# Performance work log

Measured on AMD Instinct MI355X. Metric: run time of the kernel, lower is better.

The kernel has to match this reference:

```python
import jax, jax.numpy as jnp
import numpy as np

N = 100000
E = 3200000
IN_DIM = 500
HID = 64
OUT_DIM = 40
K = 10
ALPHA = 0.1
BN_EPS = 1e-5


def setup_inputs() -> dict:
    key = jax.random.key(0)
    ks = jax.random.split(key, 10)
    x = jax.random.normal(ks[0], (N, IN_DIM), dtype=jnp.float32)
    edge_index = jax.random.randint(ks[1], (2, E), 0, N, dtype=jnp.int64)
    W1 = jax.random.normal(ks[2], (IN_DIM, HID), dtype=jnp.float32) / np.sqrt(IN_DIM)
    b1 = jnp.zeros((HID,), dtype=jnp.float32)
    bn_gamma = jnp.ones((HID,), dtype=jnp.float32)
    bn_beta = jnp.zeros((HID,), dtype=jnp.float32)
    bn_mean = jax.random.normal(ks[3], (HID,), dtype=jnp.float32) * 0.1
    bn_var = jax.random.uniform(ks[4], (HID,), dtype=jnp.float32) + 0.5
    W2 = jax.random.normal(ks[5], (HID, OUT_DIM), dtype=jnp.float32) / np.sqrt(HID)
    b2 = jnp.zeros((OUT_DIM,), dtype=jnp.float32)
    return {"x": x, "edge_index": edge_index, "W1": W1, "b1": b1,
            "bn_gamma": bn_gamma, "bn_beta": bn_beta, "bn_mean": bn_mean,
            "bn_var": bn_var, "W2": W2, "b2": b2}


def _gcn_norm(edge_index):
    # PyG gcn_norm with add_self_loops=True, symmetric normalization.
    row = jnp.concatenate([edge_index[0], jnp.arange(N, dtype=edge_index.dtype)])
    col = jnp.concatenate([edge_index[1], jnp.arange(N, dtype=edge_index.dtype)])
    deg = jax.ops.segment_sum(jnp.ones_like(col, dtype=jnp.float32), col, num_segments=N)
    dinv = jnp.where(deg > 0, jax.lax.rsqrt(deg), 0.0)
    norm = dinv[row] * dinv[col]  # [E+N]
    return row, col, norm


def _appnp(x, row, col, norm):
    h = x
    def step(xk, _):
        msg = norm[:, None] * xk[row]                       # [E+N, HID] gather
        agg = jax.ops.segment_sum(msg, col, num_segments=N)  # scatter-add
        return (1.0 - ALPHA) * agg + ALPHA * h, None
    xK, _ = jax.lax.scan(step, x, None, length=K)
    return xK


def reference(x, edge_index, W1, b1, bn_gamma, bn_beta, bn_mean, bn_var, W2, b2):
    row, col, norm = _gcn_norm(edge_index)
    h = x @ W1 + b1                                   # lin1
    h = _appnp(h, row, col, norm)                     # K-step APPNP
    h = (h - bn_mean) * jax.lax.rsqrt(bn_var + BN_EPS) * bn_gamma + bn_beta  # BN (eval)
    # dropout is identity in eval mode
    emb = h @ W2 + b2                                 # lin2
    out = jax.nn.log_softmax(emb, axis=1)
    return out, emb
```

## Files before the change

### kernel.cpp

```cpp
#include <hip/hip_runtime.h>
#include <math.h>

#define N_NODES 100000
#define N_EDGES 3200000
#define IN_DIM  500
#define HID     64
#define OUT_DIM 40
#define K_ITERS 10
#define ALPHA   0.1f
#define BN_EPS  1e-5f

#define PDIM 48
#define NBUCK 782
#define TILE_A 8192

__device__ __forceinline__ void unpack4(uint2 v, float f[4]) {
    f[0] = __uint_as_float(v.x << 16);
    f[1] = __uint_as_float(v.x & 0xffff0000u);
    f[2] = __uint_as_float(v.y << 16);
    f[3] = __uint_as_float(v.y & 0xffff0000u);
}
__device__ __forceinline__ unsigned pack2(float a, float b) {
    unsigned ua = __float_as_uint(a);
    unsigned ub = __float_as_uint(b);
    ua += ((ua >> 16) & 1u) + 0x7fffu;
    ub += ((ub >> 16) & 1u) + 0x7fffu;
    return (ua >> 16) | (ub & 0xffff0000u);
}
__device__ __forceinline__ float edge_w(unsigned e) {
    return __uint_as_float((e >> 17) << 16);
}
__device__ __forceinline__ void fma4(float4& acc, float wgt, const float f[4]) {
    acc.x = fmaf(wgt, f[0], acc.x);
    acc.y = fmaf(wgt, f[1], acc.y);
    acc.z = fmaf(wgt, f[2], acc.z);
    acc.w = fmaf(wgt, f[3], acc.w);
}


__global__ void zero_cnt_kernel(int* __restrict__ cnt) {
    int i = blockIdx.x * 256 + threadIdx.x;
    if (i < N_NODES) cnt[i] = 0;
}

__global__ void hist_kernel(const int* __restrict__ ei, int* __restrict__ cnt) {
    int e = blockIdx.x * 256 + threadIdx.x;
    if (e < N_EDGES) atomicAdd(&cnt[ei[N_EDGES + e]], 1);
}

__global__ void reduce_kernel(const int* __restrict__ cnt, int* __restrict__ psum) {
    __shared__ int s[256];
    int i = blockIdx.x * 256 + threadIdx.x;
    int v = (i < N_NODES) ? cnt[i] : 0;
    s[threadIdx.x] = v;
    __syncthreads();
    for (int off = 128; off > 0; off >>= 1) {
        if (threadIdx.x < (unsigned)off) s[threadIdx.x] += s[threadIdx.x + off];
        __syncthreads();
    }
    if (threadIdx.x == 0) psum[blockIdx.x] = s[0];
}

__global__ void scanp_kernel(const int* __restrict__ psum, int* __restrict__ pexcl,
                             int nparts) {
    __shared__ int s[512];
    int t = threadIdx.x;
    int v = (t < nparts) ? psum[t] : 0;
    s[t] = v;
    __syncthreads();
    for (int off = 1; off < 512; off <<= 1) {
        int tv = (t >= off) ? s[t - off] : 0;
        __syncthreads();
        s[t] += tv;
        __syncthreads();
    }
    if (t < nparts) pexcl[t] = s[t] - v;
}

__global__ void apply_kernel(const int* __restrict__ cnt, const int* __restrict__ pexcl,
                             int* __restrict__ rowptr, float* __restrict__ dinv) {
    __shared__ int s[256];
    int t = threadIdx.x;
    int i = blockIdx.x * 256 + t;
    int v = (i < N_NODES) ? cnt[i] : 0;
    s[t] = v;
    __syncthreads();
    for (int off = 1; off < 256; off <<= 1) {
        int tv = (t >= off) ? s[t - off] : 0;
        __syncthreads();
        s[t] += tv;
        __syncthreads();
    }
    if (i < N_NODES) {
        int excl = pexcl[blockIdx.x] + s[t] - v;
        rowptr[i] = excl;
        dinv[i] = rsqrtf((float)(v + 1));
        if (i == N_NODES - 1) rowptr[N_NODES] = excl + v;
    }
}


__global__ void bcur_init_kernel(const int* __restrict__ rowptr, int* __restrict__ bcursor) {
    int i = blockIdx.x * 256 + threadIdx.x;
    if (i < NBUCK) bcursor[i] = rowptr[i << 7];
}

__global__ __launch_bounds__(256) void bucketA_kernel(const int* __restrict__ ei,
                                                      int* __restrict__ bcursor,
                                                      unsigned* __restrict__ ebuf) {
    __shared__ int cnt[NBUCK];
    __shared__ int gbase[NBUCK];
    for (int i = threadIdx.x; i < NBUCK; i += 256) cnt[i] = 0;
    __syncthreads();
    const int e0 = blockIdx.x * TILE_A;
    const int e1 = (e0 + TILE_A < N_EDGES) ? e0 + TILE_A : N_EDGES;
    for (int e = e0 + threadIdx.x; e < e1; e += 256)
        atomicAdd(&cnt[ei[N_EDGES + e] >> 7], 1);
    __syncthreads();
    for (int i = threadIdx.x; i < NBUCK; i += 256) {
        int n = cnt[i];
        gbase[i] = (n > 0) ? atomicAdd(&bcursor[i], n) : 0;
        cnt[i] = 0;
    }
    __syncthreads();
    for (int e = e0 + threadIdx.x; e < e1; e += 256) {
        int r = ei[e];
        int c = ei[N_EDGES + e];
        int b = c >> 7;
        int rank = atomicAdd(&cnt[b], 1);
        ebuf[gbase[b] + rank] = (unsigned)r | ((unsigned)(c & 127) << 17);
    }
}

__global__ __launch_bounds__(256) void bucketB_kernel(const unsigned* __restrict__ ebuf,
                                                      const int* __restrict__ rowptr,
                                                      const float* __restrict__ dinv,
                                                      unsigned* __restrict__ ew) {
    __shared__ int lcur[128];
    __shared__ float ldinv[128];
    const int base = blockIdx.x << 7;
    const int nn = (N_NODES - base < 128) ? (N_NODES - base) : 128;
    if (threadIdx.x < (unsigned)nn) {
        lcur[threadIdx.x] = rowptr[base + threadIdx.x];
        ldinv[threadIdx.x] = dinv[base + threadIdx.x];
    }
    __syncthreads();
    const int s0 = rowptr[base];
    const int hi = (base + 128 < N_NODES) ? base + 128 : N_NODES;
    const int s1 = rowptr[hi];
    for (int p = s0 + threadIdx.x; p < s1; p += 256) {
        unsigned v = ebuf[p];
        int r = v & 0x1ffff;
        int cl = v >> 17;
        int pos = atomicAdd(&lcur[cl], 1);
        float w = dinv[r] * ldinv[cl];
        unsigned f = __float_as_uint(w) + 0x8000u;
        ew[pos] = (unsigned)r | ((f >> 16) << 17);
    }
}

__global__ void prep_kernel(const float* __restrict__ W2, const float* __restrict__ gamma,
                            const float* __restrict__ beta, const float* __restrict__ mean,
                            const float* __restrict__ var, const float* __restrict__ b1,
                            const float* __restrict__ b2, float* __restrict__ W2p,
                            float* __restrict__ c1, float* __restrict__ cbeta) {
    __shared__ float sc[64];
    __shared__ float sd[64];
    int t = threadIdx.x;
    if (t < 64) {
        float s = rsqrtf(var[t] + BN_EPS) * gamma[t];
        sc[t] = s;
        sd[t] = beta[t] - mean[t] * s;
    }
    __syncthreads();
    for (int i = t; i < 64 * OUT_DIM; i += 256) {
        int f = i / OUT_DIM;
        W2p[i] = sc[f] * W2[i];
    }
    if (t < PDIM) {
        if (t < OUT_DIM) {
            float acb = b2[t], ac1 = 0.f;
            for (int f = 0; f < 64; ++f) {
                float w2 = W2[f * OUT_DIM + t];
                acb = fmaf(sd[f], w2, acb);
                ac1 = fmaf(b1[f] * sc[f], w2, ac1);
            }
            cbeta[t] = acb;
            c1[t] = ac1;
        } else {
            c1[t] = 0.f;
        }
    }
}

__global__ __launch_bounds__(256) void wc_kernel(const float* __restrict__ W1,
                                                 const float* __restrict__ W2p,
                                                 float* __restrict__ Wc) {
    __shared__ float w2s[64 * OUT_DIM];
    for (int i = threadIdx.x; i < 64 * OUT_DIM; i += 256) w2s[i] = W2p[i];
    __syncthreads();
    int idx = blockIdx.x * 256 + threadIdx.x;
    if (idx >= IN_DIM * PDIM) return;
    int k = idx / PDIM, o = idx % PDIM;
    float a = 0.f;
    if (o < OUT_DIM) {
        const float* w1r = W1 + (size_t)k * HID;
#pragma unroll 8
        for (int f = 0; f < 64; ++f) a = fmaf(w1r[f], w2s[f * OUT_DIM + o], a);
    }
    Wc[idx] = a;
}

#define L1_M  128
#define L1_KC 20
#define L1_PITCH 132
__global__ __launch_bounds__(256) void lin1_kernel(const float* __restrict__ x,
                                                   const float* __restrict__ Wc,
                                                   const float* __restrict__ c1,
                                                   float* __restrict__ y0f,
                                                   unsigned* __restrict__ y0b) {
    __shared__ float xsT[L1_KC * L1_PITCH];
    __shared__ float wcs[L1_KC * PDIM];

    const int t = threadIdx.x;
    const int ng = t & 31;
    const int og = t >> 5;
    const int nbase = blockIdx.x * L1_M;

    const int srow = t >> 1;
    const int skb  = (t & 1) * 10;
    const int gsrc = nbase + srow;
    const int gcl  = (gsrc < N_NODES) ? gsrc : (N_NODES - 1);
    const float* xrow = x + (size_t)gcl * IN_DIM;

    float acc[4][6];
#pragma unroll
    for (int i = 0; i < 4; ++i)
#pragma unroll
        for (int j = 0; j < 6; ++j) acc[i][j] = 0.0f;

    for (int k0 = 0; k0 < IN_DIM; k0 += L1_KC) {
        __syncthreads();
#pragma unroll
        for (int u = 0; u < 5; ++u) {
            const float2 xv = *(const float2*)(xrow + k0 + skb + 2 * u);
            xsT[(skb + 2 * u) * L1_PITCH + srow]     = xv.x;
            xsT[(skb + 2 * u + 1) * L1_PITCH + srow] = xv.y;
        }
        for (int i = t; i < L1_KC * PDIM; i += 256) wcs[i] = Wc[(size_t)k0 * PDIM + i];
        __syncthreads();

#pragma unroll 4
        for (int k = 0; k < L1_KC; ++k) {
            const float4 xv = *(const float4*)&xsT[k * L1_PITCH + ng * 4];
            float w[6];
#pragma unroll
            for (int j = 0; j < 6; ++j) w[j] = wcs[k * PDIM + og * 6 + j];
            const float xr[4] = {xv.x, xv.y, xv.z, xv.w};
#pragma unroll
            for (int i = 0; i < 4; ++i)
#pragma unroll
                for (int j = 0; j < 6; ++j)
                    acc[i][j] = fmaf(xr[i], w[j], acc[i][j]);
        }
    }

    float cc[6];
#pragma unroll
    for (int j = 0; j < 6; ++j) cc[j] = c1[og * 6 + j];
#pragma unroll
    for (int i = 0; i < 4; ++i) {
        const int n = nbase + ng * 4 + i;
        if (n < N_NODES) {
            float o[6];
#pragma unroll
            for (int j = 0; j < 6; ++j) o[j] = acc[i][j] + cc[j];
            float* yf = y0f + (size_t)n * PDIM + og * 6;
            *(float2*)(yf)     = make_float2(o[0], o[1]);
            *(float2*)(yf + 2) = make_float2(o[2], o[3]);
            *(float2*)(yf + 4) = make_float2(o[4], o[5]);
            unsigned* yb = y0b + (size_t)n * (PDIM / 2) + og * 3;
            yb[0] = pack2(o[0], o[1]);
            yb[1] = pack2(o[2], o[3]);
            yb[2] = pack2(o[4], o[5]);
        }
    }
}

template <bool LAST>
__global__ __launch_bounds__(256) void appnp40_kernel(const int* __restrict__ rowptr,
                                                      const unsigned* __restrict__ ew,
                                                      const float* __restrict__ dinv,
                                                      const unsigned* __restrict__ yin,
                                                      const float* __restrict__ h,
                                                      unsigned* __restrict__ yout,
                                                      float* __restrict__ yKf) {
    const int sub   = threadIdx.x >> 4;
    const int lane4 = threadIdx.x & 15;
    const int node  = blockIdx.x * 16 + sub;
    const bool act  = lane4 < 10;

    const int beg = rowptr[node];
    const int end = rowptr[node + 1];
    float4 acc = make_float4(0.f, 0.f, 0.f, 0.f);
    int p = beg;
    for (; p + 3 < end; p += 4) {
        const unsigned e0 = ew[p], e1 = ew[p + 1], e2 = ew[p + 2], e3 = ew[p + 3];
        if (act) {
            const uint2 v0 = *(const uint2*)(yin + (size_t)(e0 & 0x1ffff) * (PDIM / 2) + lane4 * 2);
            const uint2 v1 = *(const uint2*)(yin + (size_t)(e1 & 0x1ffff) * (PDIM / 2) + lane4 * 2);
            const uint2 v2 = *(const uint2*)(yin + (size_t)(e2 & 0x1ffff) * (PDIM / 2) + lane4 * 2);
            const uint2 v3 = *(const uint2*)(yin + (size_t)(e3 & 0x1ffff) * (PDIM / 2) + lane4 * 2);
            float f0[4], f1[4], f2[4], f3[4];
            unpack4(v0, f0); unpack4(v1, f1); unpack4(v2, f2); unpack4(v3, f3);
            fma4(acc, edge_w(e0), f0);
            fma4(acc, edge_w(e1), f1);
            fma4(acc, edge_w(e2), f2);
            fma4(acc, edge_w(e3), f3);
        }
    }
    for (; p < end; ++p) {
        const unsigned e0 = ew[p];
        if (act) {
            const uint2 v0 = *(const uint2*)(yin + (size_t)(e0 & 0x1ffff) * (PDIM / 2) + lane4 * 2);
            float f0[4];
            unpack4(v0, f0);
            fma4(acc, edge_w(e0), f0);
        }
    }
    if (act) {
        const float di = dinv[node];
        const float selfw = di * di;
        const uint2 vs = *(const uint2*)(yin + (size_t)node * (PDIM / 2) + lane4 * 2);
        float fs[4];
        unpack4(vs, fs);
        const float4 hh = *(const float4*)(h + (size_t)node * PDIM + lane4 * 4);
        float4 o;
        o.x = (1.0f - ALPHA) * fmaf(selfw, fs[0], acc.x) + ALPHA * hh.x;
        o.y = (1.0f - ALPHA) * fmaf(selfw, fs[1], acc.y) + ALPHA * hh.y;
        o.z = (1.0f - ALPHA) * fmaf(selfw, fs[2], acc.z) + ALPHA * hh.z;
        o.w = (1.0f - ALPHA) * fmaf(selfw, fs[3], acc.w) + ALPHA * hh.w;
        if (LAST) {
            *(float4*)(yKf + (size_t)node * PDIM + lane4 * 4) = o;
        } else {
            uint2 w;
            w.x = pack2(o.x, o.y);
            w.y = pack2(o.z, o.w);
            *(uint2*)(yout + (size_t)node * (PDIM / 2) + lane4 * 2) = w;
        }
    }
}

__global__ __launch_bounds__(256) void final_kernel(const float* __restrict__ yKf,
                                                    const float* __restrict__ cbeta,
                                                    float* __restrict__ out_ls,
                                                    float* __restrict__ out_emb) {
    const int lane = threadIdx.x & 63;
    const int wv   = threadIdx.x >> 6;
    const int node = blockIdx.x * 4 + wv;

    float e = 0.0f;
    if (lane < OUT_DIM) e = yKf[(size_t)node * PDIM + lane] + cbeta[lane];
    float ev = (lane < OUT_DIM) ? e : -INFINITY;
    float m = ev;
#pragma unroll
    for (int off = 32; off > 0; off >>= 1) m = fmaxf(m, __shfl_xor(m, off, 64));
    float p = (lane < OUT_DIM) ? expf(ev - m) : 0.0f;
    float s = p;
#pragma unroll
    for (int off = 32; off > 0; off >>= 1) s += __shfl_xor(s, off, 64);
    if (lane < OUT_DIM) {
        float ls = ev - m - logf(s);
        out_ls[(size_t)node * OUT_DIM + lane] = ls;
        out_emb[(size_t)node * OUT_DIM + lane] = e;
    }
}


extern "C" void kernel_launch(void* const* d_in, const int* in_sizes, int n_in,
                              void* d_out, int out_size, void* d_ws, size_t ws_size,
                              hipStream_t stream) {
    const float* x     = (const float*)d_in[0];
    const int*   ei    = (const int*)d_in[1];
    const float* W1    = (const float*)d_in[2];
    const float* b1    = (const float*)d_in[3];
    const float* gamma = (const float*)d_in[4];
    const float* beta  = (const float*)d_in[5];
    const float* mean  = (const float*)d_in[6];
    const float* var   = (const float*)d_in[7];
    const float* W2    = (const float*)d_in[8];
    const float* b2    = (const float*)d_in[9];

    char* ws = (char*)d_ws;
    size_t off = 0;
    auto alloc = [&](size_t bytes) { char* p = ws + off; off += (bytes + 255) & ~(size_t)255; return p; };

    unsigned* ew     = (unsigned*)alloc((size_t)N_EDGES * 4);
    unsigned* ebuf   = (unsigned*)alloc((size_t)N_EDGES * 4);
    float*    y0f    = (float*)   alloc((size_t)N_NODES * PDIM * 4);
    float*    yKf    = (float*)   alloc((size_t)N_NODES * PDIM * 4);
    unsigned* y0b    = (unsigned*)alloc((size_t)N_NODES * (PDIM / 2) * 4);
    unsigned* ya     = (unsigned*)alloc((size_t)N_NODES * (PDIM / 2) * 4);
    unsigned* yb     = (unsigned*)alloc((size_t)N_NODES * (PDIM / 2) * 4);
    float*    Wc     = (float*)   alloc((size_t)IN_DIM * PDIM * 4);
    float*    W2p    = (float*)   alloc(64 * OUT_DIM * 4);
    float*    c1     = (float*)   alloc(PDIM * 4);
    float*    cbeta  = (float*)   alloc(OUT_DIM * 4);
    int*      cnt    = (int*)     alloc(N_NODES * 4);
    float*    dinv   = (float*)   alloc(N_NODES * 4);
    int*      rowptr = (int*)     alloc((N_NODES + 1) * 4);
    int*      bcursor= (int*)     alloc(NBUCK * 4);
    int*      psum   = (int*)     alloc(1600 * 4);
    int*      pexcl  = (int*)     alloc(1600 * 4);

    float* out_ls  = (float*)d_out;
    float* out_emb = (float*)d_out + (size_t)N_NODES * OUT_DIM;

    const int NB_N = (N_NODES + 255) / 256;
    const int NB_E = (N_EDGES + 255) / 256;
    const int NB_A = (N_EDGES + TILE_A - 1) / TILE_A;

    zero_cnt_kernel<<<NB_N, 256, 0, stream>>>(cnt);
    hist_kernel<<<NB_E, 256, 0, stream>>>(ei, cnt);
    reduce_kernel<<<NB_N, 256, 0, stream>>>(cnt, psum);
    scanp_kernel<<<1, 512, 0, stream>>>(psum, pexcl, NB_N);
    apply_kernel<<<NB_N, 256, 0, stream>>>(cnt, pexcl, rowptr, dinv);
    bcur_init_kernel<<<(NBUCK + 255) / 256, 256, 0, stream>>>(rowptr, bcursor);
    bucketA_kernel<<<NB_A, 256, 0, stream>>>(ei, bcursor, ebuf);
    bucketB_kernel<<<NBUCK, 256, 0, stream>>>(ebuf, rowptr, dinv, ew);

    prep_kernel<<<1, 256, 0, stream>>>(W2, gamma, beta, mean, var, b1, b2, W2p, c1, cbeta);
    wc_kernel<<<(IN_DIM * PDIM + 255) / 256, 256, 0, stream>>>(W1, W2p, Wc);
    lin1_kernel<<<(N_NODES + L1_M - 1) / L1_M, 256, 0, stream>>>(x, Wc, c1, y0f, y0b);

    const unsigned* cur = y0b;
    unsigned* nxt = ya;
    unsigned* buf[2] = {ya, yb};
    for (int k = 0; k < K_ITERS - 1; ++k) {
        appnp40_kernel<false><<<N_NODES / 16, 256, 0, stream>>>(rowptr, ew, dinv, cur,
                                                                y0f, nxt, nullptr);
        cur = nxt;
        nxt = buf[(k + 1) & 1];
    }
    appnp40_kernel<true><<<N_NODES / 16, 256, 0, stream>>>(rowptr, ew, dinv, cur,
                                                           y0f, nullptr, yKf);

    final_kernel<<<N_NODES / 4, 256, 0, stream>>>(yKf, cbeta, out_ls, out_emb);
}
```

Before: 1.330 ms.

## Shrink padded node features to 40 dims and use 5 lanes per node

Drops the 48-wide padding on the intermediate node-feature arrays so rows hold exactly 40 values (80 bytes in bf16), and remaps the propagation kernel to 5 lanes per node, each loading 16 bytes (8 features), with 12 nodes per wavefront. The intent is to cut gather traffic per edge and make better use of lanes in the bandwidth-bound APPNP iterations. In exchange, 4 of 64 lanes sit idle and the 80-byte rows are no longer aligned to cache-line or 32-byte boundaries. Lanes that share a node now issue edge loads together, with a bounds guard for the last block.

```diff
diff --git a/kernel.cpp b/kernel.cpp
--- a/kernel.cpp
+++ b/kernel.cpp
@@ -10,15 +10,22 @@
 #define ALPHA   0.1f
 #define BN_EPS  1e-5f
 
-#define PDIM 48
+#define WPAD 48
+#define YD   40
+#define YH   20
 #define NBUCK 782
 #define TILE_A 8192
-
-__device__ __forceinline__ void unpack4(uint2 v, float f[4]) {
+#define APG 48
+
+__device__ __forceinline__ void unpack8(uint4 v, float f[8]) {
     f[0] = __uint_as_float(v.x << 16);
     f[1] = __uint_as_float(v.x & 0xffff0000u);
     f[2] = __uint_as_float(v.y << 16);
     f[3] = __uint_as_float(v.y & 0xffff0000u);
+    f[4] = __uint_as_float(v.z << 16);
+    f[5] = __uint_as_float(v.z & 0xffff0000u);
+    f[6] = __uint_as_float(v.w << 16);
+    f[7] = __uint_as_float(v.w & 0xffff0000u);
 }
 __device__ __forceinline__ unsigned pack2(float a, float b) {
     unsigned ua = __float_as_uint(a);
@@ -30,11 +37,9 @@
 __device__ __forceinline__ float edge_w(unsigned e) {
     return __uint_as_float((e >> 17) << 16);
 }
-__device__ __forceinline__ void fma4(float4& acc, float wgt, const float f[4]) {
-    acc.x = fmaf(wgt, f[0], acc.x);
-    acc.y = fmaf(wgt, f[1], acc.y);
-    acc.z = fmaf(wgt, f[2], acc.z);
-    acc.w = fmaf(wgt, f[3], acc.w);
+__device__ __forceinline__ void fma8(float acc[8], float wgt, const float f[8]) {
+#pragma unroll
+    for (int i = 0; i < 8; ++i) acc[i] = fmaf(wgt, f[i], acc[i]);
 }
 
 
@@ -177,7 +182,7 @@
         int f = i / OUT_DIM;
         W2p[i] = sc[f] * W2[i];
     }
-    if (t < PDIM) {
+    if (t < WPAD) {
         if (t < OUT_DIM) {
             float acb = b2[t], ac1 = 0.f;
             for (int f = 0; f < 64; ++f) {
@@ -200,8 +205,8 @@
     for (int i = threadIdx.x; i < 64 * OUT_DIM; i += 256) w2s[i] = W2p[i];
     __syncthreads();
     int idx = blockIdx.x * 256 + threadIdx.x;
-    if (idx >= IN_DIM * PDIM) return;
-    int k = idx / PDIM, o = idx % PDIM;
+    if (idx >= IN_DIM * WPAD) return;
+    int k = idx / WPAD, o = idx % WPAD;
     float a = 0.f;
     if (o < OUT_DIM) {
         const float* w1r = W1 + (size_t)k * HID;
@@ -220,7 +225,7 @@
                                                    float* __restrict__ y0f,
                                                    unsigned* __restrict__ y0b) {
     __shared__ float xsT[L1_KC * L1_PITCH];
-    __shared__ float wcs[L1_KC * PDIM];
+    __shared__ float wcs[L1_KC * WPAD];
 
     const int t = threadIdx.x;
     const int ng = t & 31;
@@ -247,7 +252,7 @@
             xsT[(skb + 2 * u) * L1_PITCH + srow]     = xv.x;
             xsT[(skb + 2 * u + 1) * L1_PITCH + srow] = xv.y;
         }
-        for (int i = t; i < L1_KC * PDIM; i += 256) wcs[i] = Wc[(size_t)k0 * PDIM + i];
+        for (int i = t; i < L1_KC * WPAD; i += 256) wcs[i] = Wc[(size_t)k0 * WPAD + i];
         __syncthreads();
 
 #pragma unroll 4
@@ -255,7 +260,7 @@
             const float4 xv = *(const float4*)&xsT[k * L1_PITCH + ng * 4];
             float w[6];
 #pragma unroll
-            for (int j = 0; j < 6; ++j) w[j] = wcs[k * PDIM + og * 6 + j];
+            for (int j = 0; j < 6; ++j) w[j] = wcs[k * WPAD + og * 6 + j];
             const float xr[4] = {xv.x, xv.y, xv.z, xv.w};
 #pragma unroll
             for (int i = 0; i < 4; ++i)
@@ -275,14 +280,21 @@
             float o[6];
 #pragma unroll
             for (int j = 0; j < 6; ++j) o[j] = acc[i][j] + cc[j];
-            float* yf = y0f + (size_t)n * PDIM + og * 6;
-            *(float2*)(yf)     = make_float2(o[0], o[1]);
-            *(float2*)(yf + 2) = make_float2(o[2], o[3]);
-            *(float2*)(yf + 4) = make_float2(o[4], o[5]);
-            unsigned* yb = y0b + (size_t)n * (PDIM / 2) + og * 3;
-            yb[0] = pack2(o[0], o[1]);
-            yb[1] = pack2(o[2], o[3]);
-            yb[2] = pack2(o[4], o[5]);
+            float* yf = y0f + (size_t)n * YD + og * 6;
+            unsigned* yb = y0b + (size_t)n * YH + og * 3;
+            if (og < 6) {
+                *(float2*)(yf)     = make_float2(o[0], o[1]);
+                *(float2*)(yf + 2) = make_float2(o[2], o[3]);
+                *(float2*)(yf + 4) = make_float2(o[4], o[5]);
+                yb[0] = pack2(o[0], o[1]);
+                yb[1] = pack2(o[2], o[3]);
+                yb[2] = pack2(o[4], o[5]);
+            } else if (og == 6) {
+                *(float2*)(yf)     = make_float2(o[0], o[1]);
+                *(float2*)(yf + 2) = make_float2(o[2], o[3]);
+                yb[0] = pack2(o[0], o[1]);
+                yb[1] = pack2(o[2], o[3]);
+            }
         }
     }
 }
@@ -295,58 +307,74 @@
                                                       const float* __restrict__ h,
                                                       unsigned* __restrict__ yout,
                                                       float* __restrict__ yKf) {
-    const int sub   = threadIdx.x >> 4;
-    const int lane4 = threadIdx.x & 15;
-    const int node  = blockIdx.x * 16 + sub;
-    const bool act  = lane4 < 10;
-
-    const int beg = rowptr[node];
-    const int end = rowptr[node + 1];
-    float4 acc = make_float4(0.f, 0.f, 0.f, 0.f);
+    const int wv   = threadIdx.x >> 6;
+    const int lane = threadIdx.x & 63;
+    const int sub  = lane / 5;
+    const int dl   = lane - sub * 5;
+    const int node = blockIdx.x * APG + wv * 12 + sub;
+    const bool act = (lane < 60) && (node < N_NODES);
+    const int dl4  = dl * 4;
+
+    int beg = 0, end = 0;
+    float selfw = 0.f;
+    if (act) {
+        beg = rowptr[node];
+        end = rowptr[node + 1];
+        const float di = dinv[node];
+        selfw = di * di;
+    }
+
+    uint4 vs = make_uint4(0, 0, 0, 0);
+    float4 h0 = make_float4(0.f, 0.f, 0.f, 0.f), h1 = h0;
+    if (act) {
+        vs = *(const uint4*)(yin + (size_t)node * YH + dl4);
+        h0 = *(const float4*)(h + (size_t)node * YD + dl * 8);
+        h1 = *(const float4*)(h + (size_t)node * YD + dl * 8 + 4);
+    }
+
+    float acc[8];
+#pragma unroll
+    for (int i = 0; i < 8; ++i) acc[i] = 0.f;
+
     int p = beg;
     for (; p + 3 < end; p += 4) {
         const unsigned e0 = ew[p], e1 = ew[p + 1], e2 = ew[p + 2], e3 = ew[p + 3];
-        if (act) {
-            const uint2 v0 = *(const uint2*)(yin + (size_t)(e0 & 0x1ffff) * (PDIM / 2) + lane4 * 2);
-            const uint2 v1 = *(const uint2*)(yin + (size_t)(e1 & 0x1ffff) * (PDIM / 2) + lane4 * 2);
-            const uint2 v2 = *(const uint2*)(yin + (size_t)(e2 & 0x1ffff) * (PDIM / 2) + lane4 * 2);
-            const uint2 v3 = *(const uint2*)(yin + (size_t)(e3 & 0x1ffff) * (PDIM / 2) + lane4 * 2);
-            float f0[4], f1[4], f2[4], f3[4];
-            unpack4(v0, f0); unpack4(v1, f1); unpack4(v2, f2); unpack4(v3, f3);
-            fma4(acc, edge_w(e0), f0);
-            fma4(acc, edge_w(e1), f1);
-            fma4(acc, edge_w(e2), f2);
-            fma4(acc, edge_w(e3), f3);
-        }
+        const uint4 v0 = *(const uint4*)(yin + (size_t)(e0 & 0x1ffff) * YH + dl4);
+        const uint4 v1 = *(const uint4*)(yin + (size_t)(e1 & 0x1ffff) * YH + dl4);
+        const uint4 v2 = *(const uint4*)(yin + (size_t)(e2 & 0x1ffff) * YH + dl4);
+        const uint4 v3 = *(const uint4*)(yin + (size_t)(e3 & 0x1ffff) * YH + dl4);
+        float f[8];
+        unpack8(v0, f); fma8(acc, edge_w(e0), f);
+        unpack8(v1, f); fma8(acc, edge_w(e1), f);
+        unpack8(v2, f); fma8(acc, edge_w(e2), f);
+        unpack8(v3, f); fma8(acc, edge_w(e3), f);
     }
     for (; p < end; ++p) {
         const unsigned e0 = ew[p];
-        if (act) {
-            const uint2 v0 = *(const uint2*)(yin + (size_t)(e0 & 0x1ffff) * (PDIM / 2) + lane4 * 2);
-            float f0[4];
-            unpack4(v0, f0);
-            fma4(acc, edge_w(e0), f0);
-        }
-    }
+        const uint4 v0 = *(const uint4*)(yin + (size_t)(e0 & 0x1ffff) * YH + dl4);
+        float f[8];
+        unpack8(v0, f);
+        fma8(acc, edge_w(e0), f);
+    }
+
     if (act) {
-        const float di = dinv[node];
-        const float selfw = di * di;
-        const uint2 vs = *(const uint2*)(yin + (size_t)node * (PDIM / 2) + lane4 * 2);
-        float fs[4];
-        unpack4(vs, fs);
-        const float4 hh = *(const float4*)(h + (size_t)node * PDIM + lane4 * 4);
-        float4 o;
-        o.x = (1.0f - ALPHA) * fmaf(selfw, fs[0], acc.x) + ALPHA * hh.x;
-        o.y = (1.0f - ALPHA) * fmaf(selfw, fs[1], acc.y) + ALPHA * hh.y;
-        o.z = (1.0f - ALPHA) * fmaf(selfw, fs[2], acc.z) + ALPHA * hh.z;
-        o.w = (1.0f - ALPHA) * fmaf(selfw, fs[3], acc.w) + ALPHA * hh.w;
+        float fs[8];
+        unpack8(vs, fs);
+        const float ha[8] = {h0.x, h0.y, h0.z, h0.w, h1.x, h1.y, h1.z, h1.w};
+        float o[8];
+#pragma unroll
+        for (int i = 0; i < 8; ++i)
+            o[i] = (1.0f - ALPHA) * fmaf(selfw, fs[i], acc[i]) + ALPHA * ha[i];
         if (LAST) {
-            *(float4*)(yKf + (size_t)node * PDIM + lane4 * 4) = o;
+            *(float4*)(yKf + (size_t)node * YD + dl * 8)     = make_float4(o[0], o[1], o[2], o[3]);
+            *(float4*)(yKf + (size_t)node * YD + dl * 8 + 4) = make_float4(o[4], o[5], o[6], o[7]);
         } else {
-            uint2 w;
-            w.x = pack2(o.x, o.y);
-            w.y = pack2(o.z, o.w);
-            *(uint2*)(yout + (size_t)node * (PDIM / 2) + lane4 * 2) = w;
+            uint4 w;
+            w.x = pack2(o[0], o[1]);
+            w.y = pack2(o[2], o[3]);
+            w.z = pack2(o[4], o[5]);
+            w.w = pack2(o[6], o[7]);
+            *(uint4*)(yout + (size_t)node * YH + dl4) = w;
         }
     }
 }
@@ -360,7 +388,7 @@
     const int node = blockIdx.x * 4 + wv;
 
     float e = 0.0f;
-    if (lane < OUT_DIM) e = yKf[(size_t)node * PDIM + lane] + cbeta[lane];
+    if (lane < OUT_DIM) e = yKf[(size_t)node * YD + lane] + cbeta[lane];
     float ev = (lane < OUT_DIM) ? e : -INFINITY;
     float m = ev;
 #pragma unroll
@@ -397,14 +425,14 @@
 
     unsigned* ew     = (unsigned*)alloc((size_t)N_EDGES * 4);
     unsigned* ebuf   = (unsigned*)alloc((size_t)N_EDGES * 4);
-    float*    y0f    = (float*)   alloc((size_t)N_NODES * PDIM * 4);
-    float*    yKf    = (float*)   alloc((size_t)N_NODES * PDIM * 4);
-    unsigned* y0b    = (unsigned*)alloc((size_t)N_NODES * (PDIM / 2) * 4);
-    unsigned* ya     = (unsigned*)alloc((size_t)N_NODES * (PDIM / 2) * 4);
-    unsigned* yb     = (unsigned*)alloc((size_t)N_NODES * (PDIM / 2) * 4);
-    float*    Wc     = (float*)   alloc((size_t)IN_DIM * PDIM * 4);
+    float*    y0f    = (float*)   alloc((size_t)N_NODES * YD * 4);
+    float*    yKf    = (float*)   alloc((size_t)N_NODES * YD * 4);
+    unsigned* y0b    = (unsigned*)alloc((size_t)N_NODES * YH * 4);
+    unsigned* ya     = (unsigned*)alloc((size_t)N_NODES * YH * 4);
+    unsigned* yb     = (unsigned*)alloc((size_t)N_NODES * YH * 4);
+    float*    Wc     = (float*)   alloc((size_t)IN_DIM * WPAD * 4);
     float*    W2p    = (float*)   alloc(64 * OUT_DIM * 4);
-    float*    c1     = (float*)   alloc(PDIM * 4);
+    float*    c1     = (float*)   alloc(WPAD * 4);
     float*    cbeta  = (float*)   alloc(OUT_DIM * 4);
     int*      cnt    = (int*)     alloc(N_NODES * 4);
     float*    dinv   = (float*)   alloc(N_NODES * 4);
@@ -419,6 +447,7 @@
     const int NB_N = (N_NODES + 255) / 256;
     const int NB_E = (N_EDGES + 255) / 256;
     const int NB_A = (N_EDGES + TILE_A - 1) / TILE_A;
+    const int NB_P = (N_NODES + APG - 1) / APG;
 
     zero_cnt_kernel<<<NB_N, 256, 0, stream>>>(cnt);
     hist_kernel<<<NB_E, 256, 0, stream>>>(ei, cnt);
@@ -430,20 +459,20 @@
     bucketB_kernel<<<NBUCK, 256, 0, stream>>>(ebuf, rowptr, dinv, ew);
 
     prep_kernel<<<1, 256, 0, stream>>>(W2, gamma, beta, mean, var, b1, b2, W2p, c1, cbeta);
-    wc_kernel<<<(IN_DIM * PDIM + 255) / 256, 256, 0, stream>>>(W1, W2p, Wc);
+    wc_kernel<<<(IN_DIM * WPAD + 255) / 256, 256, 0, stream>>>(W1, W2p, Wc);
     lin1_kernel<<<(N_NODES + L1_M - 1) / L1_M, 256, 0, stream>>>(x, Wc, c1, y0f, y0b);
 
     const unsigned* cur = y0b;
     unsigned* nxt = ya;
     unsigned* buf[2] = {ya, yb};
     for (int k = 0; k < K_ITERS - 1; ++k) {
-        appnp40_kernel<false><<<N_NODES / 16, 256, 0, stream>>>(rowptr, ew, dinv, cur,
-                                                                y0f, nxt, nullptr);
+        appnp40_kernel<false><<<NB_P, 256, 0, stream>>>(rowptr, ew, dinv, cur,
+                                                        y0f, nxt, nullptr);
         cur = nxt;
         nxt = buf[(k + 1) & 1];
     }
-    appnp40_kernel<true><<<N_NODES / 16, 256, 0, stream>>>(rowptr, ew, dinv, cur,
-                                                           y0f, nullptr, yKf);
+    appnp40_kernel<true><<<NB_P, 256, 0, stream>>>(rowptr, ew, dinv, cur,
+                                                   y0f, nullptr, yKf);
 
     final_kernel<<<N_NODES / 4, 256, 0, stream>>>(yKf, cbeta, out_ls, out_emb);
 }
```

Result: no change. 1.318 ms (-0.9%).
